# Kernel tuning notes

Measured on AMD Instinct MI355X. Metric: run time of the kernel, lower is better.

The kernel has to match this reference:

```python
import jax, jax.numpy as jnp
import numpy as np

BN_EPS = 1e-5
EPS_GIN = 0.0  # pyg GINConv default eps

N_NODES = 50000
N_EDGES = 800000
D_IN = 128
D_OUT = 128


def setup_inputs() -> dict:
    key = jax.random.key(0)
    ks = jax.random.split(key, 6)
    x = jax.random.normal(ks[0], (N_NODES, D_IN), dtype=jnp.float32)
    edge_index = jax.random.randint(ks[1], (2, N_EDGES), 0, N_NODES, dtype=jnp.int32)
    # glorot-ish scale for the two Linear layers
    s1 = 1.0 / np.sqrt(D_IN)
    s2 = 1.0 / np.sqrt(D_OUT)
    W1 = jax.random.normal(ks[2], (D_IN, D_OUT), dtype=jnp.float32) * s1
    b1 = jnp.zeros((D_OUT,), dtype=jnp.float32)
    gamma = jnp.ones((D_OUT,), dtype=jnp.float32)
    beta = jnp.zeros((D_OUT,), dtype=jnp.float32)
    W2 = jax.random.normal(ks[3], (D_OUT, D_OUT), dtype=jnp.float32) * s2
    b2 = jnp.zeros((D_OUT,), dtype=jnp.float32)
    return {"x": x, "edge_index": edge_index, "W1": W1, "b1": b1,
            "gamma": gamma, "beta": beta, "W2": W2, "b2": b2}


def reference(x, edge_index, W1, b1, gamma, beta, W2, b2):
    n = x.shape[0]
    src, dst = edge_index[0], edge_index[1]  # source_to_target flow
    # scatter-add neighbor aggregation: agg[i] = sum_{(j->i)} x[j]
    agg = jax.ops.segment_sum(x[src], dst, num_segments=n)
    h = (1.0 + EPS_GIN) * x + agg  # GIN combine
    # Linear -> BatchNorm1d (training-mode batch stats, biased var) -> ReLU -> Linear
    h = h @ W1 + b1
    mean = jnp.mean(h, axis=0)
    var = jnp.var(h, axis=0)
    h = (h - mean) * jax.lax.rsqrt(var + BN_EPS) * gamma + beta
    h = jax.nn.relu(h)
    return h @ W2 + b2
```

## Files before the change

kernel.cpp:

```cpp
#include <hip/hip_runtime.h>
#include <hip/hip_bf16.h>

#define D 128
#define ELLW 64
#define BCAP 8192

typedef short bf16x8 __attribute__((ext_vector_type(8)));
typedef float f32x4 __attribute__((ext_vector_type(4)));

__device__ __forceinline__ ushort f32_to_bf16_rne(float f) {
    uint b = __float_as_uint(f);
    b += 0x7fffu + ((b >> 16) & 1u);
    return (ushort)(b >> 16);
}
__device__ __forceinline__ float bf16_bits_to_f32(ushort u) {
    return __uint_as_float(((uint)u) << 16);
}


__global__ __launch_bounds__(512) void zero_kernel(int* __restrict__ p) {
    p[threadIdx.x] = 0;
}


__global__ __launch_bounds__(1024) void prep_scatter_kernel(const float2* __restrict__ x2,
                                                            const float* __restrict__ W1,
                                                            const float* __restrict__ W2,
                                                            const int* __restrict__ src,
                                                            const int* __restrict__ dst,
                                                            uint* __restrict__ xb,
                                                            ushort* __restrict__ W1T,
                                                            ushort* __restrict__ W2T,
                                                            uint* __restrict__ part,
                                                            int* __restrict__ bcnt,
                                                            int nhalf, int m, int nbx) {
    int b = blockIdx.x, t = threadIdx.x;
    if (b < nbx) {
        int i = b * 1024 + t;
        if (i < nhalf) {
            float2 v = x2[i];
            xb[i] = ((uint)f32_to_bf16_rne(v.y) << 16) | (uint)f32_to_bf16_rne(v.x);
        }
        return;
    }
    if (b < nbx + 32) {
        int wb = b - nbx;
        const float* W = (wb < 16) ? W1 : W2;
        ushort* WT = (wb < 16) ? W1T : W2T;
        int q = wb & 15;
        int nrow = q * 8 + (t >> 7);
        int k = t & 127;
        WT[nrow * D + k] = f32_to_bf16_rne(W[k * D + nrow]);
        return;
    }
    __shared__ int hist[256];
    __shared__ int cur[256];
    if (t < 256) hist[t] = 0;
    __syncthreads();

    int base = (b - nbx - 32) * 4096;
    uint v[4];
    int bk[4];
    bool ok[4];
#pragma unroll
    for (int j = 0; j < 4; ++j) {
        int e = base + j * 1024 + t;
        ok[j] = e < m;
        bk[j] = 0;
        if (ok[j]) {
            int s_ = src[e], d_ = dst[e];
            v[j] = ((uint)s_ << 16) | (uint)d_;
            bk[j] = d_ >> 8;
            atomicAdd(&hist[bk[j]], 1);
        }
    }
    __syncthreads();
    if (t < 256) {
        int h = hist[t];
        int g = h ? atomicAdd(&bcnt[t], h) : 0;
        cur[t] = t * BCAP + g;
    }
    __syncthreads();
#pragma unroll
    for (int j = 0; j < 4; ++j) {
        if (ok[j]) {
            int pos = atomicAdd(&cur[bk[j]], 1);
            if (pos - bk[j] * BCAP < BCAP)
                part[pos] = v[j];
        }
    }
}


__global__ __launch_bounds__(512) void bucket_ell_kernel(const uint* __restrict__ part,
                                                         const int* __restrict__ bcnt,
                                                         ushort* __restrict__ col_ell,
                                                         int* __restrict__ degv, int n) {
    __shared__ int lcur[256];
    int b = blockIdx.x, t = threadIdx.x;
    if (t < 256) lcur[t] = 0;
    __syncthreads();
    int cnt = min(bcnt[b], BCAP);
    const uint* pp = part + (size_t)b * BCAP;
    for (int i = t; i < cnt; i += 512) {
        uint v = pp[i];
        int node = (int)(v & 0xffffu);
        int r = node - (b << 8);
        int s = atomicAdd(&lcur[r], 1);
        s = min(s, ELLW - 1);
        col_ell[(size_t)node * ELLW + s] = (ushort)(v >> 16);
    }
    __syncthreads();
    int node0 = b << 8;
    if (t < 256 && node0 + t < n) degv[node0 + t] = lcur[t];
}


__global__ __launch_bounds__(256) void aggregate_kernel(const uint* __restrict__ xb,
                                                        const int* __restrict__ degv,
                                                        const ushort* __restrict__ col_ell,
                                                        uint* __restrict__ h0b, int n) {
    int node = blockIdx.x * 4 + (threadIdx.x >> 6);
    if (node >= n) return;
    int lane = threadIdx.x & 63;
    uint a = xb[node * 64 + lane];
    float sx = __uint_as_float(a << 16);
    float sy = __uint_as_float(a & 0xffff0000u);
    int deg = min(degv[node], ELLW);
    const ushort* lst = col_ell + (size_t)node * ELLW;
    int e = 0;
    for (; e + 7 < deg; e += 8) {
        uint u[8];
#pragma unroll
        for (int j = 0; j < 8; ++j) u[j] = xb[(int)lst[e + j] * 64 + lane];
#pragma unroll
        for (int j = 0; j < 8; ++j) {
            sx += __uint_as_float(u[j] << 16);
            sy += __uint_as_float(u[j] & 0xffff0000u);
        }
    }
    if (e + 3 < deg) {
        uint u[4];
#pragma unroll
        for (int j = 0; j < 4; ++j) u[j] = xb[(int)lst[e + j] * 64 + lane];
#pragma unroll
        for (int j = 0; j < 4; ++j) {
            sx += __uint_as_float(u[j] << 16);
            sy += __uint_as_float(u[j] & 0xffff0000u);
        }
        e += 4;
    }
    for (; e < deg; ++e) {
        uint u = xb[(int)lst[e] * 64 + lane];
        sx += __uint_as_float(u << 16);
        sy += __uint_as_float(u & 0xffff0000u);
    }
    h0b[node * 64 + lane] = ((uint)f32_to_bf16_rne(sy) << 16) | (uint)f32_to_bf16_rne(sx);
}


template <bool BN_IN, bool STATS>
__global__ __launch_bounds__(256) void gemm_mfma_kernel(const ushort* __restrict__ inb,
                                                        const ushort* __restrict__ WT,
                                                        const float* __restrict__ bias,
                                                        void* __restrict__ outp,
                                                        const float* __restrict__ gamma,
                                                        const float* __restrict__ beta,
                                                        float* __restrict__ bn_sums,
                                                        float invn, int N) {
    __shared__ __align__(16) ushort hs[64 * D];
    __shared__ __align__(16) ushort wt[D * D];
    __shared__ float ss[2 * D];
    __shared__ float bs[D];
    __shared__ float bnl[2 * D];

    int tid = threadIdx.x;
    int row0 = blockIdx.x * 64;
    if (tid < D) bs[tid] = bias[tid];
    if (BN_IN && tid < D) {
        float mean = bn_sums[tid] * invn;
        float var = bn_sums[D + tid] * invn - mean * mean;
        float sc = gamma[tid] * rsqrtf(var + 1e-5f);
        ss[tid] = sc;
        ss[D + tid] = beta[tid] - mean * sc;
    }
    if (STATS && tid < 2 * D) bnl[tid] = 0.f;
    __syncthreads();

    char* hsb = (char*)hs;
    char* wtb = (char*)wt;

#pragma unroll
    for (int it = 0; it < 8; ++it) {
        int c = it * 256 + tid;
        int wn = c >> 4, k8 = c & 15;
        bf16x8 v = *(const bf16x8*)(WT + wn * D + k8 * 8);
        *(bf16x8*)(wtb + wn * 256 + ((k8 * 16) ^ ((wn & 7) << 4))) = v;
    }
#pragma unroll
    for (int it = 0; it < 4; ++it) {
        int c = it * 256 + tid;
        int row = c >> 4, k8 = c & 15;
        int gr = row0 + row;
        bf16x8 v;
        if (gr < N) {
            v = *(const bf16x8*)(inb + (size_t)gr * D + k8 * 8);
        } else {
#pragma unroll
            for (int j = 0; j < 8; ++j) v[j] = 0;
        }
        if (BN_IN) {
#pragma unroll
            for (int j = 0; j < 8; ++j) {
                int k = k8 * 8 + j;
                float f = bf16_bits_to_f32((ushort)v[j]);
                f = fmaxf(f * ss[k] + ss[D + k], 0.f);
                v[j] = (short)f32_to_bf16_rne(f);
            }
        }
        *(bf16x8*)(hsb + row * 256 + ((k8 * 16) ^ ((row & 7) << 4))) = v;
    }
    __syncthreads();

    int w = tid >> 6, l = tid & 63;
    int lrow = l & 15, lk = l >> 4;

    f32x4 acc[8];
#pragma unroll
    for (int f = 0; f < 8; ++f) acc[f] = (f32x4){0.f, 0.f, 0.f, 0.f};

    bf16x8 afr[4];
    int arow = w * 16 + lrow;
#pragma unroll
    for (int t = 0; t < 4; ++t)
        afr[t] = *(const bf16x8*)(hsb + arow * 256 + ((t * 64 + lk * 16) ^ ((arow & 7) << 4)));

#pragma unroll
    for (int f = 0; f < 8; ++f) {
        int nc = f * 16 + lrow;
#pragma unroll
        for (int t = 0; t < 4; ++t) {
            bf16x8 bfr = *(const bf16x8*)(wtb + nc * 256 + ((t * 64 + lk * 16) ^ ((nc & 7) << 4)));
            acc[f] = __builtin_amdgcn_mfma_f32_16x16x32_bf16(afr[t], bfr, acc[f], 0, 0, 0);
        }
    }

    int rbase = row0 + w * 16 + lk * 4;
#pragma unroll
    for (int f = 0; f < 8; ++f) {
        int colc = f * 16 + lrow;
        float bv = bs[colc];
        float s = 0.f, q = 0.f;
#pragma unroll
        for (int r = 0; r < 4; ++r) {
            int gr = rbase + r;
            if (gr < N) {
                float v = acc[f][r] + bv;
                if (STATS) {
                    ((ushort*)outp)[(size_t)gr * D + colc] = f32_to_bf16_rne(v);
                    s += v;
                    q += v * v;
                } else {
                    ((float*)outp)[(size_t)gr * D + colc] = v;
                }
            }
        }
        if (STATS) {
            s += __shfl_xor(s, 16, 64);
            s += __shfl_xor(s, 32, 64);
            q += __shfl_xor(q, 16, 64);
            q += __shfl_xor(q, 32, 64);
            if (l < 16) {
                atomicAdd(&bnl[colc], s);
                atomicAdd(&bnl[D + colc], q);
            }
        }
    }
    if (STATS) {
        __syncthreads();
        if (tid < 2 * D) atomicAdd(&bn_sums[tid], bnl[tid]);
    }
}


extern "C" void kernel_launch(void* const* d_in, const int* in_sizes, int n_in,
                              void* d_out, int out_size, void* d_ws, size_t ws_size,
                              hipStream_t stream) {
    const float* x = (const float*)d_in[0];
    const int* edge = (const int*)d_in[1];
    const float* W1 = (const float*)d_in[2];
    const float* b1 = (const float*)d_in[3];
    const float* gamma = (const float*)d_in[4];
    const float* beta = (const float*)d_in[5];
    const float* W2 = (const float*)d_in[6];
    const float* b2 = (const float*)d_in[7];

    int n = in_sizes[0] / D;
    int m = in_sizes[1] / 2;
    const int* src = edge;
    const int* dst = edge + m;

    int nbuck = (n + 255) >> 8;

    auto al = [](size_t o) { return (o + 63) & ~(size_t)63; };
    char* ws = (char*)d_ws;
    size_t off = 0;
    uint* xb = (uint*)(ws + off);
    ushort* h1b = (ushort*)(ws + off);
    off = al(off + (size_t)n * 64 * sizeof(uint));
    ushort* col_ell = (ushort*)(ws + off); off = al(off + (size_t)n * ELLW * sizeof(ushort));
    int* degv = (int*)(ws + off);     off = al(off + (size_t)n * sizeof(int));
    uint* part = (uint*)(ws + off);   off = al(off + (size_t)nbuck * BCAP * sizeof(uint));
    int* bcnt = (int*)(ws + off);     off += 256 * sizeof(int);
    float* bn_sums = (float*)(ws + off); off = al(off + 2 * D * sizeof(float));
    ushort* W1T = (ushort*)(ws + off); off = al(off + (size_t)D * D * sizeof(ushort));
    ushort* W2T = (ushort*)(ws + off); off = al(off + (size_t)D * D * sizeof(ushort));

    uint* h0b = (uint*)d_out;

    int nbx = (n * 64 + 1023) / 1024;
    int nbs = (m + 4095) / 4096;

    zero_kernel<<<1, 512, 0, stream>>>(bcnt);
    prep_scatter_kernel<<<nbx + 32 + nbs, 1024, 0, stream>>>((const float2*)x, W1, W2, src, dst,
                                                             xb, W1T, W2T, part, bcnt, n * 64, m, nbx);
    bucket_ell_kernel<<<nbuck, 512, 0, stream>>>(part, bcnt, col_ell, degv, n);
    aggregate_kernel<<<(n + 3) / 4, 256, 0, stream>>>(xb, degv, col_ell, h0b, n);
    gemm_mfma_kernel<false, true><<<(n + 63) / 64, 256, 0, stream>>>((const ushort*)h0b, W1T, b1, h1b,
                                                                     nullptr, nullptr, bn_sums, 0.f, n);
    gemm_mfma_kernel<true, false><<<(n + 63) / 64, 256, 0, stream>>>(h1b, W2T, b2, d_out,
                                                                     gamma, beta, bn_sums,
                                                                     1.0f / (float)n, n);
}
```

Baseline: 114.7 us.

## Fuse bucket-to-ELL build, aggregation and first GEMM into one kernel

```diff
diff --git a/kernel.cpp b/kernel.cpp
--- a/kernel.cpp
+++ b/kernel.cpp
@@ -16,6 +16,8 @@
 __device__ __forceinline__ float bf16_bits_to_f32(ushort u) {
     return __uint_as_float(((uint)u) << 16);
 }
+__device__ __forceinline__ float blo(uint u) { return __uint_as_float(u << 16); }
+__device__ __forceinline__ float bhi(uint u) { return __uint_as_float(u & 0xffff0000u); }
 
 
 __global__ __launch_bounds__(512) void zero_kernel(int* __restrict__ p) {
@@ -92,99 +94,156 @@
 }
 
 
-__global__ __launch_bounds__(512) void bucket_ell_kernel(const uint* __restrict__ part,
-                                                         const int* __restrict__ bcnt,
-                                                         ushort* __restrict__ col_ell,
-                                                         int* __restrict__ degv, int n) {
-    __shared__ int lcur[256];
-    int b = blockIdx.x, t = threadIdx.x;
-    if (t < 256) lcur[t] = 0;
-    __syncthreads();
-    int cnt = min(bcnt[b], BCAP);
-    const uint* pp = part + (size_t)b * BCAP;
-    for (int i = t; i < cnt; i += 512) {
+__global__ __launch_bounds__(256) void agg_gemm1_kernel(const uint* __restrict__ xb,
+                                                        const uint* __restrict__ part,
+                                                        const int* __restrict__ bcnt,
+                                                        const ushort* __restrict__ W1T,
+                                                        const float* __restrict__ bias,
+                                                        ushort* __restrict__ h1b,
+                                                        float* __restrict__ bn_sums,
+                                                        int n) {
+    __shared__ __align__(16) ushort hs[64 * D];
+    __shared__ ushort lell[64 * ELLW];
+    __shared__ int lcur[64];
+    __shared__ float bs[D];
+    __shared__ float bnl[2 * D];
+
+    int tid = threadIdx.x;
+    int row0 = blockIdx.x * 64;
+    int bkt = row0 >> 8;
+    if (tid < 64) lcur[tid] = 0;
+    if (tid < D) bs[tid] = bias[tid];
+    if (tid < 2 * D) bnl[tid] = 0.f;
+    __syncthreads();
+
+    int cnt = min(bcnt[bkt], BCAP);
+    const uint* pp = part + (size_t)bkt * BCAP;
+    for (int i = tid; i < cnt; i += 256) {
         uint v = pp[i];
-        int node = (int)(v & 0xffffu);
-        int r = node - (b << 8);
-        int s = atomicAdd(&lcur[r], 1);
-        s = min(s, ELLW - 1);
-        col_ell[(size_t)node * ELLW + s] = (ushort)(v >> 16);
-    }
-    __syncthreads();
-    int node0 = b << 8;
-    if (t < 256 && node0 + t < n) degv[node0 + t] = lcur[t];
-}
-
-
-__global__ __launch_bounds__(256) void aggregate_kernel(const uint* __restrict__ xb,
-                                                        const int* __restrict__ degv,
-                                                        const ushort* __restrict__ col_ell,
-                                                        uint* __restrict__ h0b, int n) {
-    int node = blockIdx.x * 4 + (threadIdx.x >> 6);
-    if (node >= n) return;
-    int lane = threadIdx.x & 63;
-    uint a = xb[node * 64 + lane];
-    float sx = __uint_as_float(a << 16);
-    float sy = __uint_as_float(a & 0xffff0000u);
-    int deg = min(degv[node], ELLW);
-    const ushort* lst = col_ell + (size_t)node * ELLW;
-    int e = 0;
-    for (; e + 7 < deg; e += 8) {
-        uint u[8];
-#pragma unroll
-        for (int j = 0; j < 8; ++j) u[j] = xb[(int)lst[e + j] * 64 + lane];
-#pragma unroll
-        for (int j = 0; j < 8; ++j) {
-            sx += __uint_as_float(u[j] << 16);
-            sy += __uint_as_float(u[j] & 0xffff0000u);
-        }
-    }
-    if (e + 3 < deg) {
-        uint u[4];
-#pragma unroll
-        for (int j = 0; j < 4; ++j) u[j] = xb[(int)lst[e + j] * 64 + lane];
-#pragma unroll
-        for (int j = 0; j < 4; ++j) {
-            sx += __uint_as_float(u[j] << 16);
-            sy += __uint_as_float(u[j] & 0xffff0000u);
-        }
-        e += 4;
-    }
-    for (; e < deg; ++e) {
-        uint u = xb[(int)lst[e] * 64 + lane];
-        sx += __uint_as_float(u << 16);
-        sy += __uint_as_float(u & 0xffff0000u);
-    }
-    h0b[node * 64 + lane] = ((uint)f32_to_bf16_rne(sy) << 16) | (uint)f32_to_bf16_rne(sx);
-}
-
-
-template <bool BN_IN, bool STATS>
-__global__ __launch_bounds__(256) void gemm_mfma_kernel(const ushort* __restrict__ inb,
-                                                        const ushort* __restrict__ WT,
-                                                        const float* __restrict__ bias,
-                                                        void* __restrict__ outp,
-                                                        const float* __restrict__ gamma,
-                                                        const float* __restrict__ beta,
-                                                        float* __restrict__ bn_sums,
-                                                        float invn, int N) {
+        uint r2 = (v & 0xffffu) - (uint)row0;
+        if (r2 < 64u) {
+            int s = atomicAdd(&lcur[(int)r2], 1);
+            s = min(s, ELLW - 1);
+            lell[(int)r2 * ELLW + s] = (ushort)(v >> 16);
+        }
+    }
+    __syncthreads();
+
+    int w = tid >> 6, lane = tid & 63;
+    char* hsb = (char*)hs;
+    for (int i = 0; i < 16; ++i) {
+        int r = w * 16 + i;
+        int node = row0 + r;
+        float sx = 0.f, sy = 0.f;
+        if (node < n) {
+            uint a = xb[node * 64 + lane];
+            sx = blo(a);
+            sy = bhi(a);
+            int deg = min(lcur[r], ELLW);
+            const ushort* lst = &lell[r * ELLW];
+            int e = 0;
+            for (; e + 7 < deg; e += 8) {
+                uint u[8];
+#pragma unroll
+                for (int j = 0; j < 8; ++j) u[j] = xb[(int)lst[e + j] * 64 + lane];
+#pragma unroll
+                for (int j = 0; j < 8; ++j) { sx += blo(u[j]); sy += bhi(u[j]); }
+            }
+            if (e + 3 < deg) {
+                uint u[4];
+#pragma unroll
+                for (int j = 0; j < 4; ++j) u[j] = xb[(int)lst[e + j] * 64 + lane];
+#pragma unroll
+                for (int j = 0; j < 4; ++j) { sx += blo(u[j]); sy += bhi(u[j]); }
+                e += 4;
+            }
+            for (; e < deg; ++e) {
+                uint u = xb[(int)lst[e] * 64 + lane];
+                sx += blo(u);
+                sy += bhi(u);
+            }
+        }
+        uint o = ((uint)f32_to_bf16_rne(sy) << 16) | (uint)f32_to_bf16_rne(sx);
+        *(uint*)(hsb + r * 256 + ((((lane >> 2) << 4) ^ ((r & 7) << 4)) | ((lane & 3) << 2))) = o;
+    }
+    __syncthreads();
+
+    int l = lane;
+    int lrow = l & 15, lk = l >> 4;
+
+    f32x4 acc[8];
+#pragma unroll
+    for (int f = 0; f < 8; ++f) acc[f] = (f32x4){0.f, 0.f, 0.f, 0.f};
+
+    bf16x8 afr[4];
+    int arow = w * 16 + lrow;
+#pragma unroll
+    for (int t = 0; t < 4; ++t)
+        afr[t] = *(const bf16x8*)(hsb + arow * 256 + ((t * 64 + lk * 16) ^ ((arow & 7) << 4)));
+
+#pragma unroll
+    for (int f = 0; f < 8; ++f) {
+        int nc = f * 16 + lrow;
+#pragma unroll
+        for (int t = 0; t < 4; ++t) {
+            bf16x8 bfr = *(const bf16x8*)(W1T + nc * D + t * 32 + lk * 8);
+            acc[f] = __builtin_amdgcn_mfma_f32_16x16x32_bf16(afr[t], bfr, acc[f], 0, 0, 0);
+        }
+    }
+
+    int rbase = row0 + w * 16 + lk * 4;
+#pragma unroll
+    for (int f = 0; f < 8; ++f) {
+        int colc = f * 16 + lrow;
+        float bv = bs[colc];
+        float s = 0.f, q = 0.f;
+#pragma unroll
+        for (int r = 0; r < 4; ++r) {
+            int gr = rbase + r;
+            if (gr < n) {
+                float v = acc[f][r] + bv;
+                h1b[(size_t)gr * D + colc] = f32_to_bf16_rne(v);
+                s += v;
+                q += v * v;
+            }
+        }
+        s += __shfl_xor(s, 16, 64);
+        s += __shfl_xor(s, 32, 64);
+        q += __shfl_xor(q, 16, 64);
+        q += __shfl_xor(q, 32, 64);
+        if (l < 16) {
+            atomicAdd(&bnl[colc], s);
+            atomicAdd(&bnl[D + colc], q);
+        }
+    }
+    __syncthreads();
+    if (tid < 2 * D) atomicAdd(&bn_sums[tid], bnl[tid]);
+}
+
+
+__global__ __launch_bounds__(256) void gemm2_kernel(const ushort* __restrict__ inb,
+                                                    const ushort* __restrict__ WT,
+                                                    const float* __restrict__ bias,
+                                                    float* __restrict__ outp,
+                                                    const float* __restrict__ gamma,
+                                                    const float* __restrict__ beta,
+                                                    const float* __restrict__ bn_sums,
+                                                    float invn, int N) {
     __shared__ __align__(16) ushort hs[64 * D];
     __shared__ __align__(16) ushort wt[D * D];
     __shared__ float ss[2 * D];
     __shared__ float bs[D];
-    __shared__ float bnl[2 * D];
 
     int tid = threadIdx.x;
     int row0 = blockIdx.x * 64;
     if (tid < D) bs[tid] = bias[tid];
-    if (BN_IN && tid < D) {
+    if (tid < D) {
         float mean = bn_sums[tid] * invn;
         float var = bn_sums[D + tid] * invn - mean * mean;
         float sc = gamma[tid] * rsqrtf(var + 1e-5f);
         ss[tid] = sc;
         ss[D + tid] = beta[tid] - mean * sc;
     }
-    if (STATS && tid < 2 * D) bnl[tid] = 0.f;
     __syncthreads();
 
     char* hsb = (char*)hs;
@@ -209,14 +268,12 @@
 #pragma unroll
             for (int j = 0; j < 8; ++j) v[j] = 0;
         }
-        if (BN_IN) {
-#pragma unroll
-            for (int j = 0; j < 8; ++j) {
-                int k = k8 * 8 + j;
-                float f = bf16_bits_to_f32((ushort)v[j]);
-                f = fmaxf(f * ss[k] + ss[D + k], 0.f);
-                v[j] = (short)f32_to_bf16_rne(f);
-            }
+#pragma unroll
+        for (int j = 0; j < 8; ++j) {
+            int k = k8 * 8 + j;
+            float f = bf16_bits_to_f32((ushort)v[j]);
+            f = fmaxf(f * ss[k] + ss[D + k], 0.f);
+            v[j] = (short)f32_to_bf16_rne(f);
         }
         *(bf16x8*)(hsb + row * 256 + ((k8 * 16) ^ ((row & 7) << 4))) = v;
     }
@@ -250,35 +307,11 @@
     for (int f = 0; f < 8; ++f) {
         int colc = f * 16 + lrow;
         float bv = bs[colc];
-        float s = 0.f, q = 0.f;
 #pragma unroll
         for (int r = 0; r < 4; ++r) {
             int gr = rbase + r;
-            if (gr < N) {
-                float v = acc[f][r] + bv;
-                if (STATS) {
-                    ((ushort*)outp)[(size_t)gr * D + colc] = f32_to_bf16_rne(v);
-                    s += v;
-                    q += v * v;
-                } else {
-                    ((float*)outp)[(size_t)gr * D + colc] = v;
-                }
-            }
-        }
-        if (STATS) {
-            s += __shfl_xor(s, 16, 64);
-            s += __shfl_xor(s, 32, 64);
-            q += __shfl_xor(q, 16, 64);
-            q += __shfl_xor(q, 32, 64);
-            if (l < 16) {
-                atomicAdd(&bnl[colc], s);
-                atomicAdd(&bnl[D + colc], q);
-            }
-        }
-    }
-    if (STATS) {
-        __syncthreads();
-        if (tid < 2 * D) atomicAdd(&bn_sums[tid], bnl[tid]);
+            if (gr < N) outp[(size_t)gr * D + colc] = acc[f][r] + bv;
+        }
     }
 }
 
@@ -302,33 +335,26 @@
 
     int nbuck = (n + 255) >> 8;
 
+    uint* xb = (uint*)d_out;
+
     auto al = [](size_t o) { return (o + 63) & ~(size_t)63; };
     char* ws = (char*)d_ws;
     size_t off = 0;
-    uint* xb = (uint*)(ws + off);
-    ushort* h1b = (ushort*)(ws + off);
-    off = al(off + (size_t)n * 64 * sizeof(uint));
-    ushort* col_ell = (ushort*)(ws + off); off = al(off + (size_t)n * ELLW * sizeof(ushort));
-    int* degv = (int*)(ws + off);     off = al(off + (size_t)n * sizeof(int));
-    uint* part = (uint*)(ws + off);   off = al(off + (size_t)nbuck * BCAP * sizeof(uint));
-    int* bcnt = (int*)(ws + off);     off += 256 * sizeof(int);
+    ushort* h1b = (ushort*)(ws + off); off = al(off + (size_t)n * D * sizeof(ushort));
+    uint* part = (uint*)(ws + off);    off = al(off + (size_t)nbuck * BCAP * sizeof(uint));
+    int* bcnt = (int*)(ws + off);      off += 256 * sizeof(int);
     float* bn_sums = (float*)(ws + off); off = al(off + 2 * D * sizeof(float));
     ushort* W1T = (ushort*)(ws + off); off = al(off + (size_t)D * D * sizeof(ushort));
     ushort* W2T = (ushort*)(ws + off); off = al(off + (size_t)D * D * sizeof(ushort));
 
-    uint* h0b = (uint*)d_out;
-
     int nbx = (n * 64 + 1023) / 1024;
     int nbs = (m + 4095) / 4096;
+    int nbg = (n + 63) / 64;
 
     zero_kernel<<<1, 512, 0, stream>>>(bcnt);
     prep_scatter_kernel<<<nbx + 32 + nbs, 1024, 0, stream>>>((const float2*)x, W1, W2, src, dst,
                                                              xb, W1T, W2T, part, bcnt, n * 64, m, nbx);
-    bucket_ell_kernel<<<nbuck, 512, 0, stream>>>(part, bcnt, col_ell, degv, n);
-    aggregate_kernel<<<(n + 3) / 4, 256, 0, stream>>>(xb, degv, col_ell, h0b, n);
-    gemm_mfma_kernel<false, true><<<(n + 63) / 64, 256, 0, stream>>>((const ushort*)h0b, W1T, b1, h1b,
-                                                                     nullptr, nullptr, bn_sums, 0.f, n);
-    gemm_mfma_kernel<true, false><<<(n + 63) / 64, 256, 0, stream>>>(h1b, W2T, b2, d_out,
-                                                                     gamma, beta, bn_sums,
-                                                                     1.0f / (float)n, n);
-}
+    agg_gemm1_kernel<<<nbg, 256, 0, stream>>>(xb, part, bcnt, W1T, b1, h1b, bn_sums, n);
+    gemm2_kernel<<<nbg, 256, 0, stream>>>(h1b, W2T, b2, (float*)d_out, gamma, beta,
+                                          bn_sums, 1.0f / (float)n, n);
+}
```

After: 109.6 us. -4.5%, faster.
